# Optimization experiments

Hardware: AMD Instinct MI355X
Metric: run time of the kernel (lower is better)

Reference implementation:

```python
import jax, jax.numpy as jnp
import numpy as np

N = 4096
IN_F = 256
OUT_F = 32
H = 8
NEG_SLOPE = 0.2
EDGE_P = 0.004  # avg degree ~16


def setup_inputs() -> dict:
    key = jax.random.key(0)
    k1, k2, k3, k4, k5 = jax.random.split(key, 5)
    x = jax.random.normal(k1, (N, IN_F), dtype=jnp.float32)
    adj = jax.random.bernoulli(k2, EDGE_P, (N, N))  # bool sparse-ish adjacency
    # xavier-uniform-ish scales
    w_scale = np.sqrt(6.0 / (IN_F + OUT_F))
    a_scale = np.sqrt(6.0 / (OUT_F + 1))
    W = jax.random.uniform(k3, (H, IN_F, OUT_F), jnp.float32, -w_scale, w_scale)
    a_src = jax.random.uniform(k4, (H, OUT_F), jnp.float32, -a_scale, a_scale)
    a_dst = jax.random.uniform(k5, (H, OUT_F), jnp.float32, -a_scale, a_scale)
    bias = jnp.zeros((H * OUT_F,), dtype=jnp.float32)
    return {"x": x, "adj": adj, "W": W, "a_src": a_src, "a_dst": a_dst, "bias": bias}


def reference(x, adj, W, a_src, a_dst, bias):
    n = x.shape[0]
    # adjacency mask with self-loops, (N, N)
    mask = adj | jnp.eye(n, dtype=bool)
    # Wh: (H, N, OUT_F)
    Wh = jnp.einsum('hif,ni->hnf', W, x)
    # per-node attention logits, (H, N)
    e_src = jnp.einsum('hnf,hf->hn', Wh, a_src)
    e_dst = jnp.einsum('hnf,hf->hn', Wh, a_dst)
    # additive scores, (H, N, N): row i attends over columns j
    e = e_src[:, :, None] + e_dst[:, None, :]
    e = jnp.where(e >= 0, e, NEG_SLOPE * e)  # LeakyReLU
    e = jnp.where(mask[None], e, -jnp.inf)
    alpha = jax.nn.softmax(e, axis=-1)
    # dropout p=0.6 is a no-op in eval mode
    out = jnp.einsum('hnm,hmf->hnf', alpha, Wh)
    # concat heads: (N, H*OUT_F)
    out = jnp.transpose(out, (1, 0, 2)).reshape(n, -1)
    return out + bias
```

## Files before the change

kernel.cpp:

```cpp
#include <hip/hip_runtime.h>
#include <hip/hip_bf16.h>
#include <stdint.h>

#define N_NODES 4096
#define IN_F 256
#define OUT_F 32
#define H 8
#define HF 256
#define NPB 8
#define XPAD 14
#define MAXK 64
#define NWH 512

typedef __hip_bfloat16 bf16;
__device__ __forceinline__ float b2f(bf16 v) { return __bfloat162float(v); }

__device__ __forceinline__ int detect_f32m(const void* xv, int t) {
    uint16_t u = ((const uint16_t*)xv)[t & 63];
    bf16 v = *(bf16*)&u;
    float f = b2f(v);
    int wild = !(fabsf(f) < 100.0f);
    return __popcll(__ballot(wild)) > 4;
}

union SmemU {
    float xl[IN_F][XPAD];
    struct {
        int nbr[MAXK];
        int cnt;
        int s[3];
    } b;
};

__global__ __launch_bounds__(256) void fused_kernel(
    const void* __restrict__ xv, const void* __restrict__ Wv,
    const void* __restrict__ asv, const void* __restrict__ adv,
    const uint32_t* __restrict__ adj,
    float* __restrict__ Wh, float* __restrict__ esrc, float* __restrict__ edst,
    int* __restrict__ nbrs, int* __restrict__ cnts)
{
    __shared__ SmemU sm;
    const int t = threadIdx.x;

    if (blockIdx.x >= NWH) {
        const int i = blockIdx.x - NWH;
        const int lane = t & 63;
        if (t < 3) sm.b.s[t] = 0;
        if (t == 0) sm.b.cnt = 0;
        __syncthreads();
        int E = 0, F = 0, G = 0;
        #pragma unroll
        for (int i2 = 0; i2 < 16; ++i2) {
            uint32_t w = adj[t + i2 * 256];
            if (w >> 8) E++;
            uint32_t lo = w & 0xFFFFu, hi = w >> 16;
            if (lo == 0x3F80u || hi == 0x3F80u) F++;
            if (lo) G++;
        }
        if (E) atomicAdd(&sm.b.s[0], E);
        if (F) atomicAdd(&sm.b.s[1], F);
        if (G) atomicAdd(&sm.b.s[2], G);
        __syncthreads();
        int amode;
        {
            int Eb = sm.b.s[0], Fb = sm.b.s[1], Gb = sm.b.s[2];
            if (Eb == 0)                amode = 0;
            else if (Fb > 0 && Gb == 0) amode = 0;
            else if (Fb > 0)            amode = 1;
            else                        amode = 2;
        }
        auto wpush = [&](bool pred, int col) {
            pred = pred && (col != i);
            unsigned long long mask = __ballot(pred);
            if (mask) {
                int n = __popcll(mask);
                int base = 0;
                if (lane == 0) base = atomicAdd(&sm.b.cnt, n);
                base = __shfl(base, 0, 64);
                if (pred) {
                    int p = base + __popcll(mask & ((1ull << lane) - 1));
                    if (p < MAXK) sm.b.nbr[p] = col;
                }
            }
        };

        if (amode == 0) {
            const int4* row = (const int4*)(adj + (size_t)i * N_NODES);
            #pragma unroll
            for (int rr = 0; rr < 4; ++rr) {
                int c = t + rr * 256;
                int4 v = row[c];
                int j0 = c * 4;
                wpush(v.x != 0, j0);
                wpush(v.y != 0, j0 + 1);
                wpush(v.z != 0, j0 + 2);
                wpush(v.w != 0, j0 + 3);
            }
        } else if (amode == 1) {
            const int4* row = (const int4*)((const uint16_t*)adj + (size_t)i * N_NODES);
            #pragma unroll
            for (int rr = 0; rr < 2; ++rr) {
                int c = t + rr * 256;
                int4 v = row[c];
                int j0 = c * 8;
                uint32_t w[4] = {(uint32_t)v.x, (uint32_t)v.y, (uint32_t)v.z, (uint32_t)v.w};
                #pragma unroll
                for (int q = 0; q < 4; ++q) {
                    wpush((w[q] & 0xFFFFu) != 0, j0 + 2 * q);
                    wpush((w[q] >> 16)     != 0, j0 + 2 * q + 1);
                }
            }
        } else {
            const int4* row = (const int4*)((const uint8_t*)adj + (size_t)i * N_NODES);
            int4 v = row[t];
            int j0 = t * 16;
            uint32_t w[4] = {(uint32_t)v.x, (uint32_t)v.y, (uint32_t)v.z, (uint32_t)v.w};
            #pragma unroll
            for (int q = 0; q < 4; ++q) {
                uint32_t u = w[q]; int b0 = j0 + 4 * q;
                wpush((u & 0x000000FFu) != 0, b0);
                wpush((u & 0x0000FF00u) != 0, b0 + 1);
                wpush((u & 0x00FF0000u) != 0, b0 + 2);
                wpush((u & 0xFF000000u) != 0, b0 + 3);
            }
        }
        if (t == 0) {
            int p = atomicAdd(&sm.b.cnt, 1);
            if (p < MAXK) sm.b.nbr[p] = i;
        }
        __syncthreads();
        const int K = sm.b.cnt < MAXK ? sm.b.cnt : MAXK;
        if (t < K) nbrs[(size_t)i * MAXK + t] = sm.b.nbr[t];
        if (t == 0) cnts[i] = K;
        return;
    }

    const int f32m = detect_f32m(xv, t);
    const int n0 = blockIdx.x * NPB;

    if (f32m) {
        const float* x = (const float*)xv + (size_t)n0 * IN_F;
        #pragma unroll
        for (int r = 0; r < NPB; ++r) sm.xl[t][r] = x[(size_t)r * IN_F + t];
    } else {
        const bf16* x = (const bf16*)xv + (size_t)n0 * IN_F;
        #pragma unroll
        for (int r = 0; r < NPB; ++r) sm.xl[t][r] = b2f(x[(size_t)r * IN_F + t]);
    }
    __syncthreads();

    const int rg = t >> 6;
    const int cg = t & 63;
    const int h  = cg >> 3;
    const int f0 = (cg & 7) * 4;

    float acc[2][4];
    #pragma unroll
    for (int r = 0; r < 2; ++r)
        #pragma unroll
        for (int j = 0; j < 4; ++j) acc[r][j] = 0.f;

    if (f32m) {
        const float* Wp = (const float*)Wv + (size_t)h * IN_F * OUT_F + f0;
        #pragma unroll 8
        for (int i = 0; i < IN_F; ++i) {
            const float4 w4 = *(const float4*)&Wp[(size_t)i * OUT_F];
            const float x0 = sm.xl[i][rg * 2];
            const float x1 = sm.xl[i][rg * 2 + 1];
            acc[0][0] += x0 * w4.x; acc[0][1] += x0 * w4.y;
            acc[0][2] += x0 * w4.z; acc[0][3] += x0 * w4.w;
            acc[1][0] += x1 * w4.x; acc[1][1] += x1 * w4.y;
            acc[1][2] += x1 * w4.z; acc[1][3] += x1 * w4.w;
        }
    } else {
        const bf16* Wp = (const bf16*)Wv + (size_t)h * IN_F * OUT_F + f0;
        #pragma unroll 8
        for (int i = 0; i < IN_F; ++i) {
            const ushort4 wu = *(const ushort4*)&Wp[(size_t)i * OUT_F];
            float w0 = b2f(*(bf16*)&wu.x), w1 = b2f(*(bf16*)&wu.y);
            float w2 = b2f(*(bf16*)&wu.z), w3 = b2f(*(bf16*)&wu.w);
            const float x0 = sm.xl[i][rg * 2];
            const float x1 = sm.xl[i][rg * 2 + 1];
            acc[0][0] += x0 * w0; acc[0][1] += x0 * w1;
            acc[0][2] += x0 * w2; acc[0][3] += x0 * w3;
            acc[1][0] += x1 * w0; acc[1][1] += x1 * w1;
            acc[1][2] += x1 * w2; acc[1][3] += x1 * w3;
        }
    }

    float as0, as1, as2, as3, ad0, ad1, ad2, ad3;
    if (f32m) {
        const float4 a4 = *(const float4*)&((const float*)asv)[h * OUT_F + f0];
        const float4 b4 = *(const float4*)&((const float*)adv)[h * OUT_F + f0];
        as0 = a4.x; as1 = a4.y; as2 = a4.z; as3 = a4.w;
        ad0 = b4.x; ad1 = b4.y; ad2 = b4.z; ad3 = b4.w;
    } else {
        const ushort4 a4 = *(const ushort4*)&((const bf16*)asv)[h * OUT_F + f0];
        const ushort4 b4 = *(const ushort4*)&((const bf16*)adv)[h * OUT_F + f0];
        as0 = b2f(*(bf16*)&a4.x); as1 = b2f(*(bf16*)&a4.y);
        as2 = b2f(*(bf16*)&a4.z); as3 = b2f(*(bf16*)&a4.w);
        ad0 = b2f(*(bf16*)&b4.x); ad1 = b2f(*(bf16*)&b4.y);
        ad2 = b2f(*(bf16*)&b4.z); ad3 = b2f(*(bf16*)&b4.w);
    }

    #pragma unroll
    for (int r = 0; r < 2; ++r) {
        const int n = n0 + rg * 2 + r;
        *(float4*)&Wh[(size_t)n * HF + cg * 4] =
            make_float4(acc[r][0], acc[r][1], acc[r][2], acc[r][3]);
        float vs = acc[r][0] * as0 + acc[r][1] * as1 + acc[r][2] * as2 + acc[r][3] * as3;
        float vd = acc[r][0] * ad0 + acc[r][1] * ad1 + acc[r][2] * ad2 + acc[r][3] * ad3;
        vs += __shfl_down(vs, 4, 8); vs += __shfl_down(vs, 2, 8); vs += __shfl_down(vs, 1, 8);
        vd += __shfl_down(vd, 4, 8); vd += __shfl_down(vd, 2, 8); vd += __shfl_down(vd, 1, 8);
        if ((cg & 7) == 0) {
            esrc[(size_t)n * H + h] = vs;
            edst[(size_t)n * H + h] = vd;
        }
    }
}

__global__ __launch_bounds__(256) void gat2_kernel(
    const float* __restrict__ Wh, const float* __restrict__ esrc,
    const float* __restrict__ edst, const int* __restrict__ nbrs,
    const int* __restrict__ cnts, const void* __restrict__ xv,
    const void* __restrict__ biasv, void* __restrict__ outv)
{
    __shared__ int   nbr[MAXK];
    __shared__ float sc[MAXK * H];
    __shared__ float inv_s[H];

    const int i = blockIdx.x, t = threadIdx.x;
    const int f32m = detect_f32m(xv, t);
    const int K = min(cnts[i], MAXK);
    if (t < K) nbr[t] = nbrs[(size_t)i * MAXK + t];
    __syncthreads();

    const float* esrc_i = esrc + (size_t)i * H;
    for (int idx = t; idx < K * H; idx += 256) {
        int k = idx >> 3, h = idx & 7;
        float s = esrc_i[h] + edst[(size_t)nbr[k] * H + h];
        sc[idx] = s >= 0.f ? s : 0.2f * s;
    }
    __syncthreads();

    if (t < H) {
        float mx = -1e30f;
        for (int k = 0; k < K; ++k) mx = fmaxf(mx, sc[k * H + t]);
        float sum = 0.f;
        for (int k = 0; k < K; ++k) {
            float e = __expf(sc[k * H + t] - mx);
            sc[k * H + t] = e;
            sum += e;
        }
        inv_s[t] = 1.f / sum;
    }
    __syncthreads();

    const int h = t >> 5;
    float acc = 0.f;
    #pragma unroll 4
    for (int k = 0; k < K; ++k)
        acc += sc[k * H + h] * Wh[(size_t)nbr[k] * HF + t];

    float bias = f32m ? ((const float*)biasv)[t] : b2f(((const bf16*)biasv)[t]);
    float o = acc * inv_s[h] + bias;
    if (f32m) ((float*)outv)[(size_t)i * HF + t] = o;
    else      ((bf16*)outv)[(size_t)i * HF + t] = __float2bfloat16(o);
}

extern "C" void kernel_launch(void* const* d_in, const int* in_sizes, int n_in,
                              void* d_out, int out_size, void* d_ws, size_t ws_size,
                              hipStream_t stream) {
    const void* x     = d_in[0];
    const void* adj   = d_in[1];
    const void* W     = d_in[2];
    const void* a_src = d_in[3];
    const void* a_dst = d_in[4];
    const void* bias  = d_in[5];

    float* Wh   = (float*)((char*)d_ws + 256);
    float* esrc = Wh + (size_t)N_NODES * HF;
    float* edst = esrc + (size_t)N_NODES * H;
    int*   cnts = (int*)(edst + (size_t)N_NODES * H);
    int*   nbrs = cnts + N_NODES;

    fused_kernel<<<NWH + N_NODES, 256, 0, stream>>>(
        x, W, a_src, a_dst, (const uint32_t*)adj, Wh, esrc, edst, nbrs, cnts);
    gat2_kernel<<<N_NODES, 256, 0, stream>>>(
        Wh, esrc, edst, nbrs, cnts, x, bias, d_out);
}
```

Baseline: 133.0 us.

## Process one node per wavefront in neighbor build and aggregation kernels

Both the adjacency neighbor-list build and the attention aggregation now map one node to each 64-lane wavefront, packing four nodes per block and launching a quarter as many blocks. Wave-local counters replace shared-memory atomics in the build, and the block-wide syncs become a wave barrier there. In aggregation each lane gathers float4 slices of Wh, softmax exponentials are recomputed inline rather than stored, and bias and output use vector accesses. The aim is to cut per-block sync and launch overhead and raise memory-access width. The adjacency-format detection pass still runs redundantly in every block.

Measured after the change: 127.5 us. 1.04x faster.

```diff
diff --git a/kernel.cpp b/kernel.cpp
--- a/kernel.cpp
+++ b/kernel.cpp
@@ -11,6 +11,7 @@
 #define XPAD 14
 #define MAXK 64
 #define NWH 512
+#define NBUILD 1024
 
 typedef __hip_bfloat16 bf16;
 __device__ __forceinline__ float b2f(bf16 v) { return __bfloat162float(v); }
@@ -26,8 +27,7 @@
 union SmemU {
     float xl[IN_F][XPAD];
     struct {
-        int nbr[MAXK];
-        int cnt;
+        int nbr[4][MAXK];
         int s[3];
     } b;
 };
@@ -43,17 +43,16 @@
     const int t = threadIdx.x;
 
     if (blockIdx.x >= NWH) {
-        const int i = blockIdx.x - NWH;
-        const int lane = t & 63;
+        const int w = t >> 6, lane = t & 63;
+        const int i = (blockIdx.x - NWH) * 4 + w;
         if (t < 3) sm.b.s[t] = 0;
-        if (t == 0) sm.b.cnt = 0;
         __syncthreads();
         int E = 0, F = 0, G = 0;
         #pragma unroll
         for (int i2 = 0; i2 < 16; ++i2) {
-            uint32_t w = adj[t + i2 * 256];
-            if (w >> 8) E++;
-            uint32_t lo = w & 0xFFFFu, hi = w >> 16;
+            uint32_t wd = adj[t + i2 * 256];
+            if (wd >> 8) E++;
+            uint32_t lo = wd & 0xFFFFu, hi = wd >> 16;
             if (lo == 0x3F80u || hi == 0x3F80u) F++;
             if (lo) G++;
         }
@@ -69,18 +68,19 @@
             else if (Fb > 0)            amode = 1;
             else                        amode = 2;
         }
+        int cnt = 0;
+        int* mynbr = sm.b.nbr[w];
+        const unsigned long long lmask_lt = (lane == 63) ? ~0ull >> 1
+                                          : (1ull << lane) - 1;
         auto wpush = [&](bool pred, int col) {
             pred = pred && (col != i);
             unsigned long long mask = __ballot(pred);
             if (mask) {
-                int n = __popcll(mask);
-                int base = 0;
-                if (lane == 0) base = atomicAdd(&sm.b.cnt, n);
-                base = __shfl(base, 0, 64);
                 if (pred) {
-                    int p = base + __popcll(mask & ((1ull << lane) - 1));
-                    if (p < MAXK) sm.b.nbr[p] = col;
+                    int p = cnt + __popcll(mask & ((1ull << lane) - 1));
+                    if (p < MAXK) mynbr[p] = col;
                 }
+                cnt += __popcll(mask);
             }
         };
 
@@ -88,50 +88,62 @@
             const int4* row = (const int4*)(adj + (size_t)i * N_NODES);
             #pragma unroll
             for (int rr = 0; rr < 4; ++rr) {
-                int c = t + rr * 256;
-                int4 v = row[c];
-                int j0 = c * 4;
-                wpush(v.x != 0, j0);
-                wpush(v.y != 0, j0 + 1);
-                wpush(v.z != 0, j0 + 2);
-                wpush(v.w != 0, j0 + 3);
+                int4 v[4];
+                #pragma unroll
+                for (int q = 0; q < 4; ++q) v[q] = row[lane + (rr * 4 + q) * 64];
+                #pragma unroll
+                for (int q = 0; q < 4; ++q) {
+                    int j0 = (lane + (rr * 4 + q) * 64) * 4;
+                    wpush(v[q].x != 0, j0);
+                    wpush(v[q].y != 0, j0 + 1);
+                    wpush(v[q].z != 0, j0 + 2);
+                    wpush(v[q].w != 0, j0 + 3);
+                }
             }
         } else if (amode == 1) {
             const int4* row = (const int4*)((const uint16_t*)adj + (size_t)i * N_NODES);
             #pragma unroll
             for (int rr = 0; rr < 2; ++rr) {
-                int c = t + rr * 256;
-                int4 v = row[c];
-                int j0 = c * 8;
-                uint32_t w[4] = {(uint32_t)v.x, (uint32_t)v.y, (uint32_t)v.z, (uint32_t)v.w};
+                int4 v[4];
+                #pragma unroll
+                for (int q = 0; q < 4; ++q) v[q] = row[lane + (rr * 4 + q) * 64];
                 #pragma unroll
                 for (int q = 0; q < 4; ++q) {
-                    wpush((w[q] & 0xFFFFu) != 0, j0 + 2 * q);
-                    wpush((w[q] >> 16)     != 0, j0 + 2 * q + 1);
+                    int j0 = (lane + (rr * 4 + q) * 64) * 8;
+                    uint32_t u0 = (uint32_t)v[q].x, u1 = (uint32_t)v[q].y;
+                    uint32_t u2 = (uint32_t)v[q].z, u3 = (uint32_t)v[q].w;
+                    wpush((u0 & 0xFFFFu) != 0, j0);     wpush((u0 >> 16) != 0, j0 + 1);
+                    wpush((u1 & 0xFFFFu) != 0, j0 + 2); wpush((u1 >> 16) != 0, j0 + 3);
+                    wpush((u2 & 0xFFFFu) != 0, j0 + 4); wpush((u2 >> 16) != 0, j0 + 5);
+                    wpush((u3 & 0xFFFFu) != 0, j0 + 6); wpush((u3 >> 16) != 0, j0 + 7);
                 }
             }
         } else {
             const int4* row = (const int4*)((const uint8_t*)adj + (size_t)i * N_NODES);
-            int4 v = row[t];
-            int j0 = t * 16;
-            uint32_t w[4] = {(uint32_t)v.x, (uint32_t)v.y, (uint32_t)v.z, (uint32_t)v.w};
+            int4 v[4];
+            #pragma unroll
+            for (int q = 0; q < 4; ++q) v[q] = row[lane + q * 64];
             #pragma unroll
             for (int q = 0; q < 4; ++q) {
-                uint32_t u = w[q]; int b0 = j0 + 4 * q;
-                wpush((u & 0x000000FFu) != 0, b0);
-                wpush((u & 0x0000FF00u) != 0, b0 + 1);
-                wpush((u & 0x00FF0000u) != 0, b0 + 2);
-                wpush((u & 0xFF000000u) != 0, b0 + 3);
+                int j0 = (lane + q * 64) * 16;
+                uint32_t u[4] = {(uint32_t)v[q].x, (uint32_t)v[q].y,
+                                 (uint32_t)v[q].z, (uint32_t)v[q].w};
+                #pragma unroll
+                for (int b = 0; b < 4; ++b) {
+                    uint32_t uu = u[b]; int c0 = j0 + 4 * b;
+                    wpush((uu & 0x000000FFu) != 0, c0);
+                    wpush((uu & 0x0000FF00u) != 0, c0 + 1);
+                    wpush((uu & 0x00FF0000u) != 0, c0 + 2);
+                    wpush((uu & 0xFF000000u) != 0, c0 + 3);
+                }
             }
         }
-        if (t == 0) {
-            int p = atomicAdd(&sm.b.cnt, 1);
-            if (p < MAXK) sm.b.nbr[p] = i;
-        }
-        __syncthreads();
-        const int K = sm.b.cnt < MAXK ? sm.b.cnt : MAXK;
-        if (t < K) nbrs[(size_t)i * MAXK + t] = sm.b.nbr[t];
-        if (t == 0) cnts[i] = K;
+        if (lane == 0 && cnt < MAXK) mynbr[cnt] = i;
+        cnt += 1;
+        const int K = cnt < MAXK ? cnt : MAXK;
+        __builtin_amdgcn_wave_barrier();
+        if (lane < K) nbrs[(size_t)i * MAXK + lane] = mynbr[lane];
+        if (lane == 0) cnts[i] = K;
         return;
     }
 
@@ -225,47 +237,73 @@
     const int* __restrict__ cnts, const void* __restrict__ xv,
     const void* __restrict__ biasv, void* __restrict__ outv)
 {
-    __shared__ int   nbr[MAXK];
-    __shared__ float sc[MAXK * H];
-    __shared__ float inv_s[H];
-
-    const int i = blockIdx.x, t = threadIdx.x;
+    __shared__ float sc[4][MAXK * H];
+    __shared__ int   nbw[4][MAXK];
+
+    const int t = threadIdx.x;
+    const int w = t >> 6, lane = t & 63;
+    const int i = blockIdx.x * 4 + w;
     const int f32m = detect_f32m(xv, t);
     const int K = min(cnts[i], MAXK);
-    if (t < K) nbr[t] = nbrs[(size_t)i * MAXK + t];
+
+    if (lane < K) {
+        int j = nbrs[(size_t)i * MAXK + lane];
+        nbw[w][lane] = j;
+        const float4* e4 = (const float4*)edst;
+        const float4* s4 = (const float4*)esrc;
+        float4 ej0 = e4[j * 2], ej1 = e4[j * 2 + 1];
+        float4 si0 = s4[i * 2], si1 = s4[i * 2 + 1];
+        float lg[8] = {si0.x + ej0.x, si0.y + ej0.y, si0.z + ej0.z, si0.w + ej0.w,
+                       si1.x + ej1.x, si1.y + ej1.y, si1.z + ej1.z, si1.w + ej1.w};
+        #pragma unroll
+        for (int h = 0; h < 8; ++h) {
+            float s = lg[h];
+            sc[w][lane * 8 + h] = s >= 0.f ? s : 0.2f * s;
+        }
+    }
     __syncthreads();
 
-    const float* esrc_i = esrc + (size_t)i * H;
-    for (int idx = t; idx < K * H; idx += 256) {
-        int k = idx >> 3, h = idx & 7;
-        float s = esrc_i[h] + edst[(size_t)nbr[k] * H + h];
-        sc[idx] = s >= 0.f ? s : 0.2f * s;
-    }
-    __syncthreads();
-
-    if (t < H) {
-        float mx = -1e30f;
-        for (int k = 0; k < K; ++k) mx = fmaxf(mx, sc[k * H + t]);
+    float m = -1e30f, inv = 0.f;
+    if (lane < 8) {
+        for (int k = 0; k < K; ++k) m = fmaxf(m, sc[w][k * 8 + lane]);
         float sum = 0.f;
-        for (int k = 0; k < K; ++k) {
-            float e = __expf(sc[k * H + t] - mx);
-            sc[k * H + t] = e;
-            sum += e;
-        }
-        inv_s[t] = 1.f / sum;
-    }
-    __syncthreads();
-
-    const int h = t >> 5;
-    float acc = 0.f;
+        for (int k = 0; k < K; ++k) sum += __expf(sc[w][k * 8 + lane] - m);
+        inv = 1.f / sum;
+    }
+    const int h = lane >> 3, f0c = lane * 4;
+    const float mh  = __shfl(m, h, 64);
+    const float ivh = __shfl(inv, h, 64);
+
+    float a0 = 0.f, a1 = 0.f, a2 = 0.f, a3 = 0.f;
     #pragma unroll 4
-    for (int k = 0; k < K; ++k)
-        acc += sc[k * H + h] * Wh[(size_t)nbr[k] * HF + t];
-
-    float bias = f32m ? ((const float*)biasv)[t] : b2f(((const bf16*)biasv)[t]);
-    float o = acc * inv_s[h] + bias;
-    if (f32m) ((float*)outv)[(size_t)i * HF + t] = o;
-    else      ((bf16*)outv)[(size_t)i * HF + t] = __float2bfloat16(o);
+    for (int k = 0; k < K; ++k) {
+        float e = __expf(sc[w][k * 8 + h] - mh);
+        const float4 v = *(const float4*)&Wh[(size_t)nbw[w][k] * HF + f0c];
+        a0 += e * v.x; a1 += e * v.y; a2 += e * v.z; a3 += e * v.w;
+    }
+
+    float b0, b1, b2, b3;
+    if (f32m) {
+        const float4 b4 = ((const float4*)biasv)[lane];
+        b0 = b4.x; b1 = b4.y; b2 = b4.z; b3 = b4.w;
+    } else {
+        const ushort4 b4 = ((const ushort4*)biasv)[lane];
+        b0 = b2f(*(bf16*)&b4.x); b1 = b2f(*(bf16*)&b4.y);
+        b2 = b2f(*(bf16*)&b4.z); b3 = b2f(*(bf16*)&b4.w);
+    }
+    a0 = a0 * ivh + b0; a1 = a1 * ivh + b1;
+    a2 = a2 * ivh + b2; a3 = a3 * ivh + b3;
+
+    if (f32m) {
+        ((float4*)outv)[(size_t)i * 64 + lane] = make_float4(a0, a1, a2, a3);
+    } else {
+        bf16 h0 = __float2bfloat16(a0), h1 = __float2bfloat16(a1);
+        bf16 h2 = __float2bfloat16(a2), h3 = __float2bfloat16(a3);
+        ushort4 o;
+        o.x = *(uint16_t*)&h0; o.y = *(uint16_t*)&h1;
+        o.z = *(uint16_t*)&h2; o.w = *(uint16_t*)&h3;
+        ((ushort4*)outv)[(size_t)i * 64 + lane] = o;
+    }
 }
 
 extern "C" void kernel_launch(void* const* d_in, const int* in_sizes, int n_in,
@@ -284,8 +322,8 @@
     int*   cnts = (int*)(edst + (size_t)N_NODES * H);
     int*   nbrs = cnts + N_NODES;
 
-    fused_kernel<<<NWH + N_NODES, 256, 0, stream>>>(
+    fused_kernel<<<NWH + NBUILD, 256, 0, stream>>>(
         x, W, a_src, a_dst, (const uint32_t*)adj, Wh, esrc, edst, nbrs, cnts);
-    gat2_kernel<<<N_NODES, 256, 0, stream>>>(
+    gat2_kernel<<<N_NODES / 4, 256, 0, stream>>>(
         Wh, esrc, edst, nbrs, cnts, x, bias, d_out);
 }
```
